# Optimization experiments

Measured on AMD Instinct MI355X. Metric: run time of the kernel, lower is better.

## Reference

```python
import jax, jax.numpy as jnp
import numpy as np

NEG_SLOPE = 0.01
K = 27  # 3x3x3 kernel taps


def conv3d(x, w, b, pad):
    out = jax.lax.conv_general_dilated(
        x, w, window_strides=(1, 1, 1), padding=[(pad, pad)] * 3,
        dimension_numbers=('NCDHW', 'OIDHW', 'NCDHW'))
    return out + b[None, :, None, None, None]


def lrelu(v):
    return jnp.where(v >= 0, v, NEG_SLOPE * v)


def deform_conv3d_hw(x, offsets, w, b):
    # x: [B,C,T,H,W]; offsets: [B,2*K,T,H,W] with (dh, dw) per kernel tap;
    # depth offset is 0 ('HW' mode). Bilinear sampling in H,W, zero pad OOB.
    B, C, T, H, W = x.shape
    off = offsets.reshape(B, K, 2, T, H, W)
    dh, dw = off[:, :, 0], off[:, :, 1]  # [B,K,T,H,W]
    kidx = jnp.arange(K)
    kt = (kidx // 9)[None, :, None, None, None]
    kh = ((kidx // 3) % 3)[None, :, None, None, None]
    kw = (kidx % 3)[None, :, None, None, None]

    t_in = jnp.arange(T)[None, None, :, None, None] - 1 + kt           # int, [1,K,T,1,1]
    h_s = (jnp.arange(H)[None, None, None, :, None] - 1 + kh) + dh     # [B,K,T,H,W]
    w_s = (jnp.arange(W)[None, None, None, None, :] - 1 + kw) + dw

    t_ok = (t_in >= 0) & (t_in < T)
    t_c = jnp.clip(t_in, 0, T - 1)
    t_idx = jnp.broadcast_to(t_c, (B, K, T, H, W))
    t_ok = jnp.broadcast_to(t_ok, (B, K, T, H, W))

    h0 = jnp.floor(h_s); w0 = jnp.floor(w_s)
    fh = h_s - h0; fw = w_s - w0
    h0i = h0.astype(jnp.int32); w0i = w0.astype(jnp.int32)

    def gather_b(xb, ti, hi, wi):
        return xb[:, ti, hi, wi]  # [C,K,T,H,W]
    gather = jax.vmap(gather_b)

    cols = jnp.zeros((B, C, K, T, H, W), x.dtype)
    for ih, wgt_h in ((h0i, 1.0 - fh), (h0i + 1, fh)):
        h_ok = (ih >= 0) & (ih < H)
        ih_c = jnp.clip(ih, 0, H - 1)
        for iw, wgt_w in ((w0i, 1.0 - fw), (w0i + 1, fw)):
            w_ok = (iw >= 0) & (iw < W)
            iw_c = jnp.clip(iw, 0, W - 1)
            mask = (t_ok & h_ok & w_ok).astype(x.dtype)
            wgt = (wgt_h * wgt_w * mask)[:, None]  # [B,1,K,T,H,W]
            cols = cols + wgt * gather(x, t_idx, ih_c, iw_c)
    O = w.shape[0]
    out = jnp.einsum('bckthw,ock->bothw', cols, w.reshape(O, C, K))
    return out + b[None, :, None, None, None]


def setup_inputs() -> dict:
    key = jax.random.key(0)
    ks = jax.random.split(key, 9)
    B, Cin, Cout, T, H, W = 1, 64, 64, 8, 64, 64
    s1 = 1.0 / np.sqrt(Cin * 27)
    sr = 1.0 / np.sqrt(Cin)
    sd = 1.0 / np.sqrt(Cout * 27)
    return {
        'x': jax.random.normal(ks[0], (B, Cin, T, H, W), jnp.float32),
        'W1': jax.random.normal(ks[1], (Cout, Cin, 3, 3, 3), jnp.float32) * s1,
        'b1': jax.random.normal(ks[2], (Cout,), jnp.float32) * s1,
        'W_off': jax.random.normal(ks[3], (2 * K, Cout, 3, 3, 3), jnp.float32) * 0.01,
        'b_off': jax.random.normal(ks[4], (2 * K,), jnp.float32) * 0.01,
        'Wd': jax.random.normal(ks[5], (Cout, Cout, 3, 3, 3), jnp.float32) * sd,
        'bd': jax.random.normal(ks[6], (Cout,), jnp.float32) * sd,
        'Wr': jax.random.normal(ks[7], (Cout, Cin, 1, 1, 1), jnp.float32) * sr,
        'br': jax.random.normal(ks[8], (Cout,), jnp.float32) * sr,
    }


def reference(x, W1, b1, W_off, b_off, Wd, bd, Wr, br):
    y1 = lrelu(conv3d(x, W1, b1, pad=1))
    offsets = conv3d(y1, W_off, b_off, pad=1)          # DeformConvPack offset branch
    y2 = lrelu(deform_conv3d_hw(y1, offsets, Wd, bd))  # deformable conv, 'HW' offsets
    res = conv3d(x, Wr, br, pad=0)                     # 1x1x1 residual conv
    return y2 + res
```

## Files before the change

### kernel.cpp

```cpp
#include <hip/hip_runtime.h>
#include <hip/hip_bf16.h>

#define T_ 8
#define H_ 64
#define W_ 64
#define C_ 64
#define HW_ (H_ * W_)
#define THW_ (T_ * H_ * W_)
#define KTAPS 27
#define KDIM (C_ * KTAPS)
#define NOFF 54
#define OSTR2 58

typedef __bf16 bf16x8 __attribute__((ext_vector_type(8)));
typedef float floatx4 __attribute__((ext_vector_type(4)));

#define LGKM_BARRIER()                                        \
    do {                                                      \
        asm volatile("s_waitcnt lgkmcnt(0)" ::: "memory");    \
        __builtin_amdgcn_s_barrier();                         \
    } while (0)

#define DECODE_SWZ_CONV(bid, t, h, wh)                        \
    const int hi3_ = (bid) & 7;                               \
    const int rest_ = (bid) >> 3;                             \
    const int wh = rest_ & 1;                                 \
    const int h = hi3_ * 8 + ((rest_ >> 1) & 7);              \
    const int t = rest_ >> 4;
#define DECODE_SWZ_ROW(bid, t, h)                             \
    const int h = ((bid) & 7) * 8 + (((bid) >> 3) & 7);       \
    const int t = (bid) >> 6;

__global__ __launch_bounds__(256) void prep_tocl_kernel(
    const float* __restrict__ x, __hip_bfloat16* __restrict__ xcl,
    const float* __restrict__ w1, const float* __restrict__ woff,
    const float* __restrict__ wd, const float* __restrict__ wr,
    __hip_bfloat16* __restrict__ w1s, __hip_bfloat16* __restrict__ woffs,
    __hip_bfloat16* __restrict__ wds, __hip_bfloat16* __restrict__ wrs) {
    __shared__ float tile[64][65];
    const int tid = threadIdx.x;

    {
        int i = blockIdx.x * 256 + tid;
        if (i < C_ * KDIM) {
            int j = i & 7, lane = (i >> 3) & 63, s = (i >> 9) & 1, g16 = (i >> 10) & 3, tap = i >> 12;
            int co = g16 * 16 + (lane & 15);
            int cin = s * 32 + (lane >> 4) * 8 + j;
            int src = (co * C_ + cin) * KTAPS + tap;
            w1s[i] = __float2bfloat16(w1[src]);
            woffs[i] = (co < NOFF) ? __float2bfloat16(woff[src]) : __float2bfloat16(0.f);
            wds[i] = __float2bfloat16(wd[src]);
        }
        if (i < C_ * C_) {
            int j = i & 7, lane = (i >> 3) & 63, s = (i >> 9) & 1, g16 = i >> 10;
            int co = g16 * 16 + (lane & 15);
            int cin = s * 32 + (lane >> 4) * 8 + j;
            wrs[i] = __float2bfloat16(wr[co * C_ + cin]);
        }
    }

    const int pos0 = blockIdx.x * 64;
    for (int i = tid; i < 4096; i += 256) {
        int ch = i >> 6, p = i & 63;
        tile[ch][p] = x[ch * THW_ + pos0 + p];
    }
    __syncthreads();
    for (int i = tid; i < 4096; i += 256) {
        int p = i >> 6, ch = i & 63;
        xcl[(pos0 + p) * C_ + ch] = __float2bfloat16(tile[ch][p]);
    }
}

__global__ __launch_bounds__(256) void conv_stream_kernel(
    const __hip_bfloat16* __restrict__ in_cl,
    const __hip_bfloat16* __restrict__ wTs,
    const float* __restrict__ bias,
    __hip_bfloat16* __restrict__ out_cl_b16) {
    __shared__ __hip_bfloat16 ts[32 * 72];

    const int tid = threadIdx.x;
    const int wv = tid >> 6;
    const int lane = tid & 63;
    const int l15 = lane & 15;
    const int quad = lane >> 4;
    DECODE_SWZ_CONV(blockIdx.x, t, h, wh)
    const int w0 = wh * 32;
    const int pg = wv >> 1;
    const int chf = wv & 1;
    const int wpos = w0 + pg * 16 + l15;
    const int posbase = t * HW_ + h * W_;

    floatx4 acc0 = (floatx4){0.f, 0.f, 0.f, 0.f};
    floatx4 acc1 = (floatx4){0.f, 0.f, 0.f, 0.f};
    const bf16x8 z = {};
    const __hip_bfloat16* wb = wTs + chf * 2048 + lane * 8;

    const int ktlo = (t == 0) ? 1 : 0;
    const int kthi = (t == T_ - 1) ? 2 : 3;

    for (int kt = ktlo; kt < kthi; ++kt) {
        const int t_in = t - 1 + kt;
#pragma unroll 1
        for (int kh = 0; kh < 3; ++kh) {
            const int h_in = h - 1 + kh;
            if ((unsigned)h_in >= H_) continue;
            const int rowbase = t_in * HW_ + h_in * W_;
#pragma unroll
            for (int kw = 0; kw < 3; ++kw) {
                const int tap = kt * 9 + kh * 3 + kw;
                const int w_in = wpos - 1 + kw;
                const bool v = (unsigned)w_in < W_;
                const int wc = v ? w_in : 0;
                const __hip_bfloat16* ap = in_cl + (rowbase + wc) * C_ + quad * 8;
                bf16x8 a0 = *(const bf16x8*)(ap);
                bf16x8 a1 = *(const bf16x8*)(ap + 32);
                a0 = v ? a0 : z;
                a1 = v ? a1 : z;
                const __hip_bfloat16* bp = wb + tap * 4096;
                const bf16x8 b00 = *(const bf16x8*)(bp);
                const bf16x8 b01 = *(const bf16x8*)(bp + 512);
                const bf16x8 b10 = *(const bf16x8*)(bp + 1024);
                const bf16x8 b11 = *(const bf16x8*)(bp + 1536);
                acc0 = __builtin_amdgcn_mfma_f32_16x16x32_bf16(a0, b00, acc0, 0, 0, 0);
                acc0 = __builtin_amdgcn_mfma_f32_16x16x32_bf16(a1, b01, acc0, 0, 0, 0);
                acc1 = __builtin_amdgcn_mfma_f32_16x16x32_bf16(a0, b10, acc1, 0, 0, 0);
                acc1 = __builtin_amdgcn_mfma_f32_16x16x32_bf16(a1, b11, acc1, 0, 0, 0);
            }
        }
    }

    const int n0 = chf * 32 + l15;
    const float bv0 = bias[n0], bv1 = bias[n0 + 16];
#pragma unroll
    for (int r = 0; r < 4; ++r) {
        const int p = pg * 16 + quad * 4 + r;
        float v0 = acc0[r] + bv0;
        v0 = (v0 >= 0.f) ? v0 : 0.01f * v0;
        float v1 = acc1[r] + bv1;
        v1 = (v1 >= 0.f) ? v1 : 0.01f * v1;
        ts[p * 72 + n0] = __float2bfloat16(v0);
        ts[p * 72 + n0 + 16] = __float2bfloat16(v1);
    }
    __syncthreads();
    {
        const int p = tid >> 3, ck = tid & 7;
        const uint4 v4 = *(const uint4*)&ts[p * 72 + ck * 8];
        *(uint4*)&out_cl_b16[(posbase + w0 + p) * C_ + ck * 8] = v4;
    }
}

struct G2 {
    bf16x8 a[4];
    bf16x8 b[4];
    float w00, w01, w10, w11;
};

__global__ __launch_bounds__(256) void deform_fused_kernel(
    const __hip_bfloat16* __restrict__ y1b,
    const __hip_bfloat16* __restrict__ woffs, const float* __restrict__ boff,
    const __hip_bfloat16* __restrict__ wds, const float* __restrict__ bd,
    const __hip_bfloat16* __restrict__ xclb, const __hip_bfloat16* __restrict__ wrs,
    const float* __restrict__ br, float* __restrict__ out) {
    __shared__ __hip_bfloat16 win[6 * 64 * 64];
    __shared__ float offs[4][16][OSTR2];

    const int tid = threadIdx.x;
    const int wv = tid >> 6;
    const int lane = tid & 63;
    const int l15 = lane & 15;
    const int quad = lane >> 4;
    DECODE_SWZ_ROW(blockIdx.x, t, h)
    const int posbase = t * HW_ + h * W_;
    const int pw = wv * 16 + l15;

    const int ktlo = (t == 0) ? 1 : 0;
    const int kthi = (t == T_ - 1) ? 2 : 3;

    {
        floatx4 oacc[4];
#pragma unroll
        for (int g = 0; g < 4; ++g) oacc[g] = (floatx4){0.f, 0.f, 0.f, 0.f};
        const bf16x8 z = {};

        for (int kt = ktlo; kt < kthi; ++kt) {
            const int t_in = t - 1 + kt;
#pragma unroll 1
            for (int kh = 0; kh < 3; ++kh) {
                const int h_in = h - 1 + kh;
                if ((unsigned)h_in >= H_) continue;
                const int rowbase = t_in * HW_ + h_in * W_;
#pragma unroll
                for (int kw = 0; kw < 3; ++kw) {
                    const int tap = kt * 9 + kh * 3 + kw;
                    const int w_in = pw - 1 + kw;
                    const bool v = (unsigned)w_in < W_;
                    const int wc = v ? w_in : 0;
                    const __hip_bfloat16* ap = y1b + (rowbase + wc) * C_ + quad * 8;
                    bf16x8 a0 = *(const bf16x8*)(ap);
                    bf16x8 a1 = *(const bf16x8*)(ap + 32);
                    a0 = v ? a0 : z;
                    a1 = v ? a1 : z;
                    const __hip_bfloat16* op = woffs + tap * 4096 + lane * 8;
#pragma unroll
                    for (int g = 0; g < 4; ++g) {
                        const bf16x8 b0 = *(const bf16x8*)(op + g * 1024);
                        const bf16x8 b1 = *(const bf16x8*)(op + g * 1024 + 512);
                        oacc[g] = __builtin_amdgcn_mfma_f32_16x16x32_bf16(a0, b0, oacc[g], 0, 0, 0);
                        oacc[g] = __builtin_amdgcn_mfma_f32_16x16x32_bf16(a1, b1, oacc[g], 0, 0, 0);
                    }
                }
            }
        }
#pragma unroll
        for (int g = 0; g < 4; ++g) {
            const int idx = g * 16 + l15;
            if (idx < NOFF) {
                const float bo = boff[idx];
#pragma unroll
                for (int r = 0; r < 4; ++r)
                    offs[wv][quad * 4 + r][idx] = oacc[g][r] + bo;
            }
        }
    }
    asm volatile("s_waitcnt lgkmcnt(0)" ::: "memory");

    floatx4 acc[4], racc[4];
#pragma unroll
    for (int g = 0; g < 4; ++g) {
        acc[g] = (floatx4){0.f, 0.f, 0.f, 0.f};
        racc[g] = (floatx4){0.f, 0.f, 0.f, 0.f};
    }

    {
        const __hip_bfloat16* ap = xclb + (posbase + pw) * C_ + quad * 8;
        const bf16x8 ra0 = *(const bf16x8*)(ap);
        const bf16x8 ra1 = *(const bf16x8*)(ap + 32);
        const __hip_bfloat16* q = wrs + lane * 8;
#pragma unroll
        for (int g = 0; g < 4; ++g) {
            const bf16x8 r0 = *(const bf16x8*)(q + g * 1024);
            const bf16x8 r1 = *(const bf16x8*)(q + g * 1024 + 512);
            racc[g] = __builtin_amdgcn_mfma_f32_16x16x32_bf16(ra0, r0, racc[g], 0, 0, 0);
            racc[g] = __builtin_amdgcn_mfma_f32_16x16x32_bf16(ra1, r1, racc[g], 0, 0, 0);
        }
    }

    auto load_off = [&](int k, float& dh, float& dw) {
        dh = offs[wv][l15][2 * k];
        dw = offs[wv][l15][2 * k + 1];
    };
    auto rdwin = [&](int rr, int cc, int chunk) -> bf16x8 {
        const int u = (rr * 64 + cc) * 8 + (chunk ^ (cc & 7));
        return *(const bf16x8*)((const char*)win + u * 16);
    };
    auto gatherW = [&](int k, float dh, float dw, G2& g) {
        const int kh = (k / 3) % 3, kw = k % 3;
        const float hs = (float)(h - 1 + kh) + dh;
        const float wsv = (float)(pw - 1 + kw) + dw;
        const float h0f = floorf(hs), w0f = floorf(wsv);
        const float fh = hs - h0f, fw = wsv - w0f;
        const int h0i = (int)h0f, w0i = (int)w0f;
        const int h1i = h0i + 1, w1i = w0i + 1;
        const float m_h0 = ((unsigned)h0i < H_) ? 1.f : 0.f;
        const float m_h1 = ((unsigned)h1i < H_) ? 1.f : 0.f;
        const float m_w0 = ((unsigned)w0i < W_) ? 1.f : 0.f;
        const float m_w1 = ((unsigned)w1i < W_) ? 1.f : 0.f;
        g.w00 = (1.f - fh) * (1.f - fw) * m_h0 * m_w0;
        g.w01 = (1.f - fh) * fw * m_h0 * m_w1;
        g.w10 = fh * (1.f - fw) * m_h1 * m_w0;
        g.w11 = fh * fw * m_h1 * m_w1;
        const int w0c = min(max(w0i, 0), W_ - 1);
        const int w1c = min(max(w1i, 0), W_ - 1);
        const int rh = h0i - (h - 2);
        if ((unsigned)rh <= 4u) {
            g.a[0] = rdwin(rh, w0c, quad);      g.b[0] = rdwin(rh, w0c, quad + 4);
            g.a[1] = rdwin(rh, w1c, quad);      g.b[1] = rdwin(rh, w1c, quad + 4);
            g.a[2] = rdwin(rh + 1, w0c, quad);  g.b[2] = rdwin(rh + 1, w0c, quad + 4);
            g.a[3] = rdwin(rh + 1, w1c, quad);  g.b[3] = rdwin(rh + 1, w1c, quad + 4);
        } else {
            const int h0c = min(max(h0i, 0), H_ - 1);
            const int h1c = min(max(h1i, 0), H_ - 1);
            const int tb = (t - 1 + k / 9) * HW_;
            const __hip_bfloat16* p00 = y1b + (tb + h0c * W_ + w0c) * C_ + quad * 8;
            const __hip_bfloat16* p01 = y1b + (tb + h0c * W_ + w1c) * C_ + quad * 8;
            const __hip_bfloat16* p10 = y1b + (tb + h1c * W_ + w0c) * C_ + quad * 8;
            const __hip_bfloat16* p11 = y1b + (tb + h1c * W_ + w1c) * C_ + quad * 8;
            g.a[0] = *(const bf16x8*)(p00);  g.b[0] = *(const bf16x8*)(p00 + 32);
            g.a[1] = *(const bf16x8*)(p01);  g.b[1] = *(const bf16x8*)(p01 + 32);
            g.a[2] = *(const bf16x8*)(p10);  g.b[2] = *(const bf16x8*)(p10 + 32);
            g.a[3] = *(const bf16x8*)(p11);  g.b[3] = *(const bf16x8*)(p11 + 32);
        }
    };
    auto blend2 = [&](const G2& g, bf16x8& lo, bf16x8& hi) {
        union U { bf16x8 v; __hip_bfloat16 e[8]; };
        U c0, c1, c2, c3, r;
        c0.v = g.a[0]; c1.v = g.a[1]; c2.v = g.a[2]; c3.v = g.a[3];
#pragma unroll
        for (int j = 0; j < 8; ++j) {
            float f = g.w00 * __bfloat162float(c0.e[j]) + g.w01 * __bfloat162float(c1.e[j]) +
                      g.w10 * __bfloat162float(c2.e[j]) + g.w11 * __bfloat162float(c3.e[j]);
            r.e[j] = __float2bfloat16(f);
        }
        lo = r.v;
        c0.v = g.b[0]; c1.v = g.b[1]; c2.v = g.b[2]; c3.v = g.b[3];
#pragma unroll
        for (int j = 0; j < 8; ++j) {
            float f = g.w00 * __bfloat162float(c0.e[j]) + g.w01 * __bfloat162float(c1.e[j]) +
                      g.w10 * __bfloat162float(c2.e[j]) + g.w11 * __bfloat162float(c3.e[j]);
            r.e[j] = __float2bfloat16(f);
        }
        hi = r.v;
    };
    auto tapMFMA = [&](int k, const bf16x8& lo, const bf16x8& hi) {
        const __hip_bfloat16* q = wds + k * 4096 + lane * 8;
#pragma unroll
        for (int g = 0; g < 4; ++g) {
            const bf16x8 b0 = *(const bf16x8*)(q + g * 1024);
            const bf16x8 b1 = *(const bf16x8*)(q + g * 1024 + 512);
            acc[g] = __builtin_amdgcn_mfma_f32_16x16x32_bf16(lo, b0, acc[g], 0, 0, 0);
            acc[g] = __builtin_amdgcn_mfma_f32_16x16x32_bf16(hi, b1, acc[g], 0, 0, 0);
        }
    };

    G2 gA, gB;
#pragma unroll 1
    for (int kt = ktlo; kt < kthi; ++kt) {
        const int tin = t - 1 + kt;
        const int kg = kt * 9;

        LGKM_BARRIER();
        for (int i = tid; i < 6 * 64 * 8; i += 256) {
            const int rh = i >> 9;
            const int rem = i & 511;
            const int rw = rem >> 3;
            const int cc = rem & 7;
            const int hsrc = min(max(h - 2 + rh, 0), H_ - 1);
            const int u = (rh * 64 + rw) * 8 + (cc ^ (rw & 7));
            *(bf16x8*)((char*)win + u * 16) =
                *(const bf16x8*)&y1b[(tin * HW_ + hsrc * W_ + rw) * C_ + cc * 8];
        }
        LGKM_BARRIER();

        {
            float dh, dw;
            load_off(kg, dh, dw);
            gatherW(kg, dh, dw, gA);
        }
        int k = kg;
        for (; k + 1 < kg + 9; k += 2) {
            {
                float dh, dw;
                load_off(k + 1, dh, dw);
                gatherW(k + 1, dh, dw, gB);
                bf16x8 lo, hi;
                blend2(gA, lo, hi);
                tapMFMA(k, lo, hi);
            }
            {
                if (k + 2 < kg + 9) {
                    float dh, dw;
                    load_off(k + 2, dh, dw);
                    gatherW(k + 2, dh, dw, gA);
                }
                bf16x8 lo, hi;
                blend2(gB, lo, hi);
                tapMFMA(k + 1, lo, hi);
            }
        }
        {
            bf16x8 lo, hi;
            blend2(gA, lo, hi);
            tapMFMA(k, lo, hi);
        }
    }

#pragma unroll
    for (int g = 0; g < 4; ++g) {
        const int n = g * 16 + l15;
        const float bdv = bd[n], brv = br[n];
        floatx4 o;
#pragma unroll
        for (int r = 0; r < 4; ++r) {
            float v = acc[g][r] + bdv;
            v = (v >= 0.f) ? v : 0.01f * v;
            o[r] = v + racc[g][r] + brv;
        }
        *(floatx4*)&out[n * THW_ + posbase + wv * 16 + quad * 4] = o;
    }
}

extern "C" void kernel_launch(void* const* d_in, const int* in_sizes, int n_in,
                              void* d_out, int out_size, void* d_ws, size_t ws_size,
                              hipStream_t stream) {
    const float* x    = (const float*)d_in[0];
    const float* W1   = (const float*)d_in[1];
    const float* b1   = (const float*)d_in[2];
    const float* Woff = (const float*)d_in[3];
    const float* boff = (const float*)d_in[4];
    const float* Wd   = (const float*)d_in[5];
    const float* bd   = (const float*)d_in[6];
    const float* Wr   = (const float*)d_in[7];
    const float* br   = (const float*)d_in[8];
    float* out = (float*)d_out;

    float* ws = (float*)d_ws;
    __hip_bfloat16* xclb  = (__hip_bfloat16*)(ws);
    __hip_bfloat16* y1b   = (__hip_bfloat16*)(ws + 1048576);
    __hip_bfloat16* w1s   = (__hip_bfloat16*)(ws + 2097152);
    __hip_bfloat16* woffs = (__hip_bfloat16*)(ws + 2152448);
    __hip_bfloat16* wdsb  = (__hip_bfloat16*)(ws + 2207744);
    __hip_bfloat16* wrsb  = (__hip_bfloat16*)(ws + 2263040);

    prep_tocl_kernel<<<THW_ / 64, 256, 0, stream>>>(
        x, xclb, W1, Woff, Wd, Wr, w1s, woffs, wdsb, wrsb);

    conv_stream_kernel<<<dim3(T_ * H_ * 2), 256, 0, stream>>>(
        xclb, w1s, b1, y1b);

    deform_fused_kernel<<<dim3(T_ * H_), 256, 0, stream>>>(
        y1b, woffs, boff, wdsb, bd, xclb, wrsb, br, out);
}
```

Baseline: 177.9 us.

## Split deform kernel into half-row blocks with output-channel halves per wave

The fused deformable kernel now launches twice as many blocks, each covering 32 pixels of a row. Waves are split into two pixel groups by two output-channel halves, so each wave does half the MFMAs per tap. The shared window shrinks to 5 rows by 38 columns, and offsets are stored in bf16 in shared memory. This buys more parallelism and smaller LDS for higher occupancy, at the cost of duplicated offset-conv and gather work across the channel-half waves. Offset precision also drops, which may move sample positions slightly.

```diff
diff --git a/kernel.cpp b/kernel.cpp
--- a/kernel.cpp
+++ b/kernel.cpp
@@ -10,7 +10,9 @@
 #define KTAPS 27
 #define KDIM (C_ * KTAPS)
 #define NOFF 54
-#define OSTR2 58
+#define WR_ 5
+#define WC_ 38
+#define WCP 40
 
 typedef __bf16 bf16x8 __attribute__((ext_vector_type(8)));
 typedef float floatx4 __attribute__((ext_vector_type(4)));
@@ -27,9 +29,6 @@
     const int wh = rest_ & 1;                                 \
     const int h = hi3_ * 8 + ((rest_ >> 1) & 7);              \
     const int t = rest_ >> 4;
-#define DECODE_SWZ_ROW(bid, t, h)                             \
-    const int h = ((bid) & 7) * 8 + (((bid) >> 3) & 7);       \
-    const int t = (bid) >> 6;
 
 __global__ __launch_bounds__(256) void prep_tocl_kernel(
     const float* __restrict__ x, __hip_bfloat16* __restrict__ xcl,
@@ -161,26 +160,29 @@
     const __hip_bfloat16* __restrict__ wds, const float* __restrict__ bd,
     const __hip_bfloat16* __restrict__ xclb, const __hip_bfloat16* __restrict__ wrs,
     const float* __restrict__ br, float* __restrict__ out) {
-    __shared__ __hip_bfloat16 win[6 * 64 * 64];
-    __shared__ float offs[4][16][OSTR2];
+    __shared__ __hip_bfloat16 win[WR_ * WCP * C_];
+    __shared__ __hip_bfloat16 offs[2][16][58];
 
     const int tid = threadIdx.x;
     const int wv = tid >> 6;
     const int lane = tid & 63;
     const int l15 = lane & 15;
     const int quad = lane >> 4;
-    DECODE_SWZ_ROW(blockIdx.x, t, h)
-    const int posbase = t * HW_ + h * W_;
-    const int pw = wv * 16 + l15;
+    DECODE_SWZ_CONV(blockIdx.x, t, h, wh)
+    const int w0 = wh * 32;
+    const int pg = wv & 1;
+    const int oh = wv >> 1;
+    const int pw = w0 + pg * 16 + l15;
 
     const int ktlo = (t == 0) ? 1 : 0;
     const int kthi = (t == T_ - 1) ? 2 : 3;
 
     {
-        floatx4 oacc[4];
-#pragma unroll
-        for (int g = 0; g < 4; ++g) oacc[g] = (floatx4){0.f, 0.f, 0.f, 0.f};
+        const int chf = oh;
+        floatx4 oa0 = (floatx4){0.f, 0.f, 0.f, 0.f};
+        floatx4 oa1 = (floatx4){0.f, 0.f, 0.f, 0.f};
         const bf16x8 z = {};
+        const __hip_bfloat16* wb = woffs + chf * 2048 + lane * 8;
 
         for (int kt = ktlo; kt < kthi; ++kt) {
             const int t_in = t - 1 + kt;
@@ -200,44 +202,44 @@
                     bf16x8 a1 = *(const bf16x8*)(ap + 32);
                     a0 = v ? a0 : z;
                     a1 = v ? a1 : z;
-                    const __hip_bfloat16* op = woffs + tap * 4096 + lane * 8;
-#pragma unroll
-                    for (int g = 0; g < 4; ++g) {
-                        const bf16x8 b0 = *(const bf16x8*)(op + g * 1024);
-                        const bf16x8 b1 = *(const bf16x8*)(op + g * 1024 + 512);
-                        oacc[g] = __builtin_amdgcn_mfma_f32_16x16x32_bf16(a0, b0, oacc[g], 0, 0, 0);
-                        oacc[g] = __builtin_amdgcn_mfma_f32_16x16x32_bf16(a1, b1, oacc[g], 0, 0, 0);
-                    }
+                    const __hip_bfloat16* bp = wb + tap * 4096;
+                    const bf16x8 b00 = *(const bf16x8*)(bp);
+                    const bf16x8 b01 = *(const bf16x8*)(bp + 512);
+                    const bf16x8 b10 = *(const bf16x8*)(bp + 1024);
+                    const bf16x8 b11 = *(const bf16x8*)(bp + 1536);
+                    oa0 = __builtin_amdgcn_mfma_f32_16x16x32_bf16(a0, b00, oa0, 0, 0, 0);
+                    oa0 = __builtin_amdgcn_mfma_f32_16x16x32_bf16(a1, b01, oa0, 0, 0, 0);
+                    oa1 = __builtin_amdgcn_mfma_f32_16x16x32_bf16(a0, b10, oa1, 0, 0, 0);
+                    oa1 = __builtin_amdgcn_mfma_f32_16x16x32_bf16(a1, b11, oa1, 0, 0, 0);
                 }
             }
         }
-#pragma unroll
-        for (int g = 0; g < 4; ++g) {
-            const int idx = g * 16 + l15;
-            if (idx < NOFF) {
-                const float bo = boff[idx];
-#pragma unroll
-                for (int r = 0; r < 4; ++r)
-                    offs[wv][quad * 4 + r][idx] = oacc[g][r] + bo;
-            }
-        }
-    }
-    asm volatile("s_waitcnt lgkmcnt(0)" ::: "memory");
-
-    floatx4 acc[4], racc[4];
-#pragma unroll
-    for (int g = 0; g < 4; ++g) {
+        const int n0 = chf * 32 + l15;
+        const float bv0 = boff[n0];
+        const float bv1 = (n0 + 16 < NOFF) ? boff[n0 + 16] : 0.f;
+#pragma unroll
+        for (int r = 0; r < 4; ++r) {
+            const int p = quad * 4 + r;
+            offs[pg][p][n0] = __float2bfloat16(oa0[r] + bv0);
+            if (n0 + 16 < NOFF) offs[pg][p][n0 + 16] = __float2bfloat16(oa1[r] + bv1);
+        }
+    }
+    LGKM_BARRIER();
+
+    floatx4 acc[2], racc[2];
+#pragma unroll
+    for (int g = 0; g < 2; ++g) {
         acc[g] = (floatx4){0.f, 0.f, 0.f, 0.f};
         racc[g] = (floatx4){0.f, 0.f, 0.f, 0.f};
     }
 
     {
-        const __hip_bfloat16* ap = xclb + (posbase + pw) * C_ + quad * 8;
+        const __hip_bfloat16* ap = xclb + (t * HW_ + h * W_ + pw) * C_ + quad * 8;
         const bf16x8 ra0 = *(const bf16x8*)(ap);
         const bf16x8 ra1 = *(const bf16x8*)(ap + 32);
-        const __hip_bfloat16* q = wrs + lane * 8;
-#pragma unroll
-        for (int g = 0; g < 4; ++g) {
+        const __hip_bfloat16* q = wrs + oh * 2048 + lane * 8;
+#pragma unroll
+        for (int g = 0; g < 2; ++g) {
             const bf16x8 r0 = *(const bf16x8*)(q + g * 1024);
             const bf16x8 r1 = *(const bf16x8*)(q + g * 1024 + 512);
             racc[g] = __builtin_amdgcn_mfma_f32_16x16x32_bf16(ra0, r0, racc[g], 0, 0, 0);
@@ -246,11 +248,13 @@
     }
 
     auto load_off = [&](int k, float& dh, float& dw) {
-        dh = offs[wv][l15][2 * k];
-        dw = offs[wv][l15][2 * k + 1];
+        union { uint u; __hip_bfloat16 b[2]; } cv;
+        cv.u = *(const uint*)&offs[pg][l15][2 * k];
+        dh = __bfloat162float(cv.b[0]);
+        dw = __bfloat162float(cv.b[1]);
     };
     auto rdwin = [&](int rr, int cc, int chunk) -> bf16x8 {
-        const int u = (rr * 64 + cc) * 8 + (chunk ^ (cc & 7));
+        const int u = (rr * WCP + cc) * 8 + (chunk ^ (cc & 7));
         return *(const bf16x8*)((const char*)win + u * 16);
     };
     auto gatherW = [&](int k, float dh, float dw, G2& g) {
@@ -272,11 +276,13 @@
         const int w0c = min(max(w0i, 0), W_ - 1);
         const int w1c = min(max(w1i, 0), W_ - 1);
         const int rh = h0i - (h - 2);
-        if ((unsigned)rh <= 4u) {
-            g.a[0] = rdwin(rh, w0c, quad);      g.b[0] = rdwin(rh, w0c, quad + 4);
-            g.a[1] = rdwin(rh, w1c, quad);      g.b[1] = rdwin(rh, w1c, quad + 4);
-            g.a[2] = rdwin(rh + 1, w0c, quad);  g.b[2] = rdwin(rh + 1, w0c, quad + 4);
-            g.a[3] = rdwin(rh + 1, w1c, quad);  g.b[3] = rdwin(rh + 1, w1c, quad + 4);
+        const int rw0 = w0c - (w0 - 2);
+        const int rw1 = w1c - (w0 - 2);
+        if ((unsigned)rh <= 3u && (unsigned)rw0 <= 37u && (unsigned)rw1 <= 37u) {
+            g.a[0] = rdwin(rh, rw0, quad);      g.b[0] = rdwin(rh, rw0, quad + 4);
+            g.a[1] = rdwin(rh, rw1, quad);      g.b[1] = rdwin(rh, rw1, quad + 4);
+            g.a[2] = rdwin(rh + 1, rw0, quad);  g.b[2] = rdwin(rh + 1, rw0, quad + 4);
+            g.a[3] = rdwin(rh + 1, rw1, quad);  g.b[3] = rdwin(rh + 1, rw1, quad + 4);
         } else {
             const int h0c = min(max(h0i, 0), H_ - 1);
             const int h1c = min(max(h1i, 0), H_ - 1);
@@ -312,9 +318,9 @@
         hi = r.v;
     };
     auto tapMFMA = [&](int k, const bf16x8& lo, const bf16x8& hi) {
-        const __hip_bfloat16* q = wds + k * 4096 + lane * 8;
-#pragma unroll
-        for (int g = 0; g < 4; ++g) {
+        const __hip_bfloat16* q = wds + k * 4096 + oh * 2048 + lane * 8;
+#pragma unroll
+        for (int g = 0; g < 2; ++g) {
             const bf16x8 b0 = *(const bf16x8*)(q + g * 1024);
             const bf16x8 b1 = *(const bf16x8*)(q + g * 1024 + 512);
             acc[g] = __builtin_amdgcn_mfma_f32_16x16x32_bf16(lo, b0, acc[g], 0, 0, 0);
@@ -329,15 +335,16 @@
         const int kg = kt * 9;
 
         LGKM_BARRIER();
-        for (int i = tid; i < 6 * 64 * 8; i += 256) {
-            const int rh = i >> 9;
-            const int rem = i & 511;
+        for (int i = tid; i < WR_ * WC_ * 8; i += 256) {
+            const int rh = i / (WC_ * 8);
+            const int rem = i - rh * (WC_ * 8);
             const int rw = rem >> 3;
             const int cc = rem & 7;
             const int hsrc = min(max(h - 2 + rh, 0), H_ - 1);
-            const int u = (rh * 64 + rw) * 8 + (cc ^ (rw & 7));
+            const int wsrc = min(max(w0 - 2 + rw, 0), W_ - 1);
+            const int u = (rh * WCP + rw) * 8 + (cc ^ (rw & 7));
             *(bf16x8*)((char*)win + u * 16) =
-                *(const bf16x8*)&y1b[(tin * HW_ + hsrc * W_ + rw) * C_ + cc * 8];
+                *(const bf16x8*)&y1b[(tin * HW_ + hsrc * W_ + wsrc) * C_ + cc * 8];
         }
         LGKM_BARRIER();
 
@@ -375,8 +382,8 @@
     }
 
 #pragma unroll
-    for (int g = 0; g < 4; ++g) {
-        const int n = g * 16 + l15;
+    for (int g = 0; g < 2; ++g) {
+        const int n = oh * 32 + g * 16 + l15;
         const float bdv = bd[n], brv = br[n];
         floatx4 o;
 #pragma unroll
@@ -385,7 +392,7 @@
             v = (v >= 0.f) ? v : 0.01f * v;
             o[r] = v + racc[g][r] + brv;
         }
-        *(floatx4*)&out[n * THW_ + posbase + wv * 16 + quad * 4] = o;
+        *(floatx4*)&out[n * THW_ + t * HW_ + h * W_ + w0 + pg * 16 + quad * 4] = o;
     }
 }
 
@@ -417,6 +424,6 @@
     conv_stream_kernel<<<dim3(T_ * H_ * 2), 256, 0, stream>>>(
         xclb, w1s, b1, y1b);
 
-    deform_fused_kernel<<<dim3(T_ * H_), 256, 0, stream>>>(
+    deform_fused_kernel<<<dim3(T_ * H_ * 2), 256, 0, stream>>>(
         y1b, woffs, boff, wdsb, bd, xclb, wrsb, br, out);
 }
```

After: 191.3 us. +7.5%, slower.
